# Optimization experiments

Measured on AMD Instinct MI355X. Metric: run time of the kernel, lower is better.

## Reference

```python
import jax, jax.numpy as jnp
import numpy as np
from itertools import permutations

BLOCK = 64  # GroupLinear block_size


def _dist_bucket_table():
    # replicates self.distance: log2-style bucketing of token distances [0,1024)
    t = np.zeros(1024, dtype=np.int32)
    for i, th in enumerate([2, 4, 8, 16, 32, 64, 128, 256, 512]):
        t[th:] = i + 1
    return jnp.asarray(t)


def setup_inputs() -> dict:
    key = jax.random.key(0)
    ks = jax.random.split(key, 12)
    B, S, H, NH = 4, 512, 768, 12
    E, TAG, TE, TD, R = 24, 7, 20, 20, 97
    DIN = 2 * H + TE + TD
    hidden_state = jax.random.normal(ks[0], (B, S, H), jnp.float32)
    attention = jax.random.uniform(ks[1], (B, NH, S, S), jnp.float32)
    attention_mask = jnp.ones((B, S), jnp.float32)
    head = jnp.sort(jax.random.randint(ks[2], (B, E), 0, S), axis=-1)
    tail = jnp.sort(jax.random.randint(ks[3], (B, E), 0, S), axis=-1)
    entity_type = jax.random.randint(ks[4], (B, E), 0, TAG)
    type_table = jax.random.normal(ks[5], (TAG, TE), jnp.float32) * 0.02
    dis_table = jax.random.normal(ks[6], (20, TD), jnp.float32) * 0.02
    Wh = jax.random.normal(ks[7], (DIN, H), jnp.float32) * (1.0 / np.sqrt(DIN))
    bh = jnp.zeros((H,), jnp.float32)
    Wt = jax.random.normal(ks[8], (DIN, H), jnp.float32) * (1.0 / np.sqrt(DIN))
    bt = jnp.zeros((H,), jnp.float32)
    # GroupLinear weight reshaped to [n_blocks, BLOCK, BLOCK, R]
    clsW = jax.random.normal(ks[9], (H // BLOCK, BLOCK, BLOCK, R), jnp.float32) * (1.0 / np.sqrt(H * BLOCK))
    clsb = jnp.zeros((R,), jnp.float32)
    return dict(hidden_state=hidden_state, attention=attention,
                attention_mask=attention_mask, head=head, tail=tail,
                entity_type=entity_type, type_table=type_table,
                dis_table=dis_table, Wh=Wh, bh=bh, Wt=Wt, bt=bt,
                clsW=clsW, clsb=clsb)


def reference(hidden_state, attention, attention_mask, head, tail, entity_type,
              type_table, dis_table, Wh, bh, Wt, bt, clsW, clsb):
    E = head.shape[1]
    hts = jnp.asarray(list(permutations(range(E), 2)), dtype=jnp.int32)  # [P,2]
    i0, i1 = hts[:, 0], hts[:, 1]
    dtab = _dist_bucket_table()
    att = attention.sum(axis=1)  # [B,S,S] sum over heads

    def per_sample(h, a, m, hd, tl, et):
        # h:[S,H] a:[S,S] m:[S] hd,tl,et:[E]
        ent_feat = (h[hd] + h[tl]) * 0.5          # [E,H]
        ent_att = (a[hd] + a[tl]) * 0.5           # [E,S]
        ent_tf = type_table[et]                   # [E,TE]
        head_f, tail_f = ent_feat[i0], ent_feat[i1]      # [P,H]
        ht_att = ent_att[i0] * ent_att[i1] * m[None, :]  # [P,S]
        head_ty, tail_ty = ent_tf[i0], ent_tf[i1]        # [P,TE]
        d = dtab[jnp.abs(tl[i0] - hd[i1])]               # [P]
        ht_dist = dis_table[d]                           # [P,TD]
        ht_att = ht_att / (ht_att.sum(-1, keepdims=True) + 1e-20)
        ht_info = ht_att @ h                             # [P,H]
        all_h = jnp.concatenate([head_f, ht_info, head_ty, ht_dist], axis=-1)
        all_t = jnp.concatenate([tail_f, ht_info, tail_ty, ht_dist], axis=-1)
        return all_h, all_t

    all_h, all_t = jax.vmap(per_sample)(hidden_state, att, attention_mask,
                                        head, tail, entity_type)
    all_h = all_h.reshape(-1, all_h.shape[-1])  # [B*P, DIN]
    all_t = all_t.reshape(-1, all_t.shape[-1])
    h1 = jnp.tanh(all_h @ Wh + bh)              # [L,H]
    t1 = jnp.tanh(all_t @ Wt + bt)
    L, H = h1.shape
    nb = H // BLOCK
    x1 = h1.reshape(L, nb, BLOCK)
    x2 = t1.reshape(L, nb, BLOCK)
    # GroupLinear: per-block outer product then linear, fused as einsum
    logits = jnp.einsum('lnb,lnc,nbcr->lr', x1, x2, clsW) + clsb  # [L,R]
    return logits
```

## Files before the change

### kernel.cpp

```cpp
#include <hip/hip_runtime.h>
#include <hip/hip_bf16.h>
#include <math.h>

#define B_ 4
#define S_ 512
#define H_ 768
#define NH_ 12
#define E_ 24
#define TE_ 20
#define TD_ 20
#define R_ 97
#define DIN_ 1576
#define KPAD_ 1600
#define KS_MLP 50
#define KS_HTI 16
#define P_ 552
#define L_ 2208
#define NB_ 12
#define NF_ 7

typedef __bf16 bf16x8 __attribute__((ext_vector_type(8)));
typedef float f32x4 __attribute__((ext_vector_type(4)));

__device__ __forceinline__ unsigned short f2bf(float f) {
  union { float f; unsigned u; } c; c.f = f;
  unsigned r = c.u + 0x7FFF + ((c.u >> 16) & 1);
  return (unsigned short)(r >> 16);
}
__device__ __forceinline__ float bf2f(unsigned short b) {
  union { unsigned u; float f; } c; c.u = ((unsigned)b) << 16;
  return c.f;
}
__device__ __forceinline__ unsigned pk2(float a, float b) {
  return (unsigned)f2bf(a) | ((unsigned)f2bf(b) << 16);
}
__device__ __forceinline__ void gload_lds16(const uint4* g, uint4* l) {
  __builtin_amdgcn_global_load_lds(
      (const __attribute__((address_space(1))) unsigned*)(const void*)g,
      (__attribute__((address_space(3))) unsigned*)(void*)l, 16, 0, 0);
}

__global__ void ent_prep(const float* __restrict__ attn, const float* __restrict__ hs,
                         const int* __restrict__ head, const int* __restrict__ tail,
                         float* __restrict__ ent_att, float* __restrict__ ent_feat) {
  int be = blockIdx.x;
  int b = be / E_;
  int hd = head[be], tl = tail[be];
  int tid = threadIdx.x;
  const float* abase = attn + (size_t)b * NH_ * S_ * S_;
  for (int s = tid; s < S_; s += 256) {
    float acc = 0.f;
#pragma unroll
    for (int nh = 0; nh < NH_; ++nh) {
      const float* ap = abase + (size_t)nh * S_ * S_;
      acc += ap[(size_t)hd * S_ + s] + ap[(size_t)tl * S_ + s];
    }
    ent_att[(size_t)be * S_ + s] = 0.5f * acc;
  }
  const float* hb = hs + (size_t)b * S_ * H_;
  for (int k = tid; k < H_; k += 256) {
    ent_feat[(size_t)be * H_ + k] = 0.5f * (hb[(size_t)hd * H_ + k] + hb[(size_t)tl * H_ + k]);
  }
}

__global__ void pair_att(const float* __restrict__ ent_att, const float* __restrict__ mask,
                         const int* __restrict__ head, const int* __restrict__ tail,
                         const int* __restrict__ etype,
                         float* __restrict__ ht_att, int* __restrict__ meta) {
  int l = blockIdx.x;
  int b = l / P_, p = l % P_;
  int i0 = p / (E_ - 1), rem = p % (E_ - 1);
  int i1 = rem + (rem >= i0 ? 1 : 0);
  int tid = threadIdx.x;
  if (tid == 0) {
    meta[0 * L_ + l] = b * E_ + i0;
    meta[1 * L_ + l] = b * E_ + i1;
    meta[2 * L_ + l] = etype[b * E_ + i0];
    meta[3 * L_ + l] = etype[b * E_ + i1];
    int d = abs(tail[b * E_ + i0] - head[b * E_ + i1]);
    int bk = (d >= 2) + (d >= 4) + (d >= 8) + (d >= 16) + (d >= 32) +
             (d >= 64) + (d >= 128) + (d >= 256) + (d >= 512);
    meta[4 * L_ + l] = bk;
  }
  const float* a0 = ent_att + (size_t)(b * E_ + i0) * S_;
  const float* a1 = ent_att + (size_t)(b * E_ + i1) * S_;
  const float* m = mask + (size_t)b * S_;
  float v0 = a0[tid] * a1[tid] * m[tid];
  float v1 = a0[tid + 256] * a1[tid + 256] * m[tid + 256];
  float loc = v0 + v1;
  for (int o = 32; o > 0; o >>= 1) loc += __shfl_down(loc, o, 64);
  __shared__ float red[4];
  if ((tid & 63) == 0) red[tid >> 6] = loc;
  __syncthreads();
  float tot = red[0] + red[1] + red[2] + red[3];
  float inv = 1.f / (tot + 1e-20f);
  ht_att[(size_t)l * S_ + tid] = v0 * inv;
  ht_att[(size_t)l * S_ + tid + 256] = v1 * inv;
}

__global__ void pack_hs(const float* __restrict__ hs, uint4* __restrict__ hsP) {
  int u = blockIdx.x * 256 + threadIdx.x;
  if (u >= B_ * KS_HTI * 48 * 64) return;
  int lane = u & 63;
  int t = u >> 6;
  int nt16 = t % 48;
  int t2 = t / 48;
  int ks = t2 % KS_HTI;
  int b = t2 / KS_HTI;
  int n = nt16 * 16 + (lane & 15);
  int k0 = ks * 32 + ((lane >> 4) << 3);
  const float* src = hs + (size_t)b * S_ * H_;
  unsigned w[4];
#pragma unroll
  for (int q = 0; q < 4; ++q) {
    int k = k0 + 2 * q;
    w[q] = pk2(src[(size_t)k * H_ + n], src[(size_t)(k + 1) * H_ + n]);
  }
  uint4 o; o.x = w[0]; o.y = w[1]; o.z = w[2]; o.w = w[3];
  hsP[u] = o;
}

__global__ void pack_Wmlp(const float* __restrict__ Wh, const float* __restrict__ Wt,
                          uint4* __restrict__ WpH, uint4* __restrict__ WpT) {
  int u = blockIdx.x * 256 + threadIdx.x;
  if (u >= KS_MLP * 48 * 64) return;
  const float* W = blockIdx.y ? Wt : Wh;
  uint4* Wp = blockIdx.y ? WpT : WpH;
  int lane = u & 63;
  int t = u >> 6;
  int nt16 = t % 48;
  int ks = t / 48;
  int n = nt16 * 16 + (lane & 15);
  int k0 = ks * 32 + ((lane >> 4) << 3);
  unsigned w[4];
#pragma unroll
  for (int q = 0; q < 4; ++q) {
    int k = k0 + 2 * q;
    float v0 = (k < DIN_) ? W[(size_t)k * H_ + n] : 0.f;
    float v1 = (k + 1 < DIN_) ? W[(size_t)(k + 1) * H_ + n] : 0.f;
    w[q] = pk2(v0, v1);
  }
  uint4 o; o.x = w[0]; o.y = w[1]; o.z = w[2]; o.w = w[3];
  Wp[u] = o;
}

__global__ __launch_bounds__(256) void htinfo_mfma(
    const float* __restrict__ htatt, const uint4* __restrict__ hsP,
    float* __restrict__ htinfo) {
  int b = blockIdx.z;
  int m0 = blockIdx.x * 64;
  int n0 = blockIdx.y * 64;
  int tid = threadIdx.x;
  int wave = tid >> 6, lane = tid & 63;
  int wm = wave & 1, wn = wave >> 1;
  __shared__ __align__(16) unsigned short Ash[2][2048];
  __shared__ __align__(16) uint4 Bsh[2][256];

  int amt = tid >> 6, alane = tid & 63;
  int arow = m0 + amt * 16 + (alane & 15);
  bool rowok = arow < P_;
  const float* ap = htatt + ((size_t)b * P_ + (rowok ? arow : 0)) * S_;
  int akoff = (alane >> 4) << 3;
  int nt0 = n0 >> 4;

  f32x4 acc[2][2];
#pragma unroll
  for (int i = 0; i < 2; ++i)
#pragma unroll
    for (int j = 0; j < 2; ++j) acc[i][j] = (f32x4){0.f, 0.f, 0.f, 0.f};

  auto stageB = [&](int ks, int buf) {
    const uint4* gs = hsP + ((size_t)(b * KS_HTI + ks) * 48 + nt0 + wave) * 64 + lane;
    gload_lds16(gs, &Bsh[buf][wave * 64]);
  };
  auto gatherA = [&](int ks, uint4& d) {
    if (!rowok) { d.x = d.y = d.z = d.w = 0; return; }
    int k = ks * 32 + akoff;
    float4 v0 = *(const float4*)(ap + k);
    float4 v1 = *(const float4*)(ap + k + 4);
    d.x = pk2(v0.x, v0.y); d.y = pk2(v0.z, v0.w);
    d.z = pk2(v1.x, v1.y); d.w = pk2(v1.z, v1.w);
  };

  {
    stageB(0, 0);
    uint4 aU; gatherA(0, aU);
    *(uint4*)&Ash[0][tid * 8] = aU;
  }
  __syncthreads();

  for (int ks = 0; ks < KS_HTI; ++ks) {
    int cur = ks & 1, nxt = cur ^ 1;
    bool more = (ks + 1 < KS_HTI);
    uint4 aN;
    if (more) {
      stageB(ks + 1, nxt);
      gatherA(ks + 1, aN);
    }
    bf16x8 af[2], bf[2];
#pragma unroll
    for (int mf = 0; mf < 2; ++mf)
      af[mf] = *(const bf16x8*)&Ash[cur][((wm * 2 + mf) * 64 + lane) * 8];
#pragma unroll
    for (int nf = 0; nf < 2; ++nf)
      bf[nf] = *(const bf16x8*)&Bsh[cur][(wn * 2 + nf) * 64 + lane];
#pragma unroll
    for (int nf = 0; nf < 2; ++nf)
#pragma unroll
      for (int mf = 0; mf < 2; ++mf)
        acc[mf][nf] = __builtin_amdgcn_mfma_f32_16x16x32_bf16(af[mf], bf[nf], acc[mf][nf], 0, 0, 0);
    if (more)
      *(uint4*)&Ash[nxt][tid * 8] = aN;
    __syncthreads();
  }

#pragma unroll
  for (int mf = 0; mf < 2; ++mf)
#pragma unroll
    for (int nf = 0; nf < 2; ++nf) {
      int n = n0 + (wn * 2 + nf) * 16 + (lane & 15);
#pragma unroll
      for (int reg = 0; reg < 4; ++reg) {
        int l = m0 + (wm * 2 + mf) * 16 + ((lane >> 4) << 2) + reg;
        if (l < P_)
          htinfo[((size_t)b * P_ + l) * H_ + n] = acc[mf][nf][reg];
      }
    }
}

__global__ __launch_bounds__(256) void mlp_mfma(
    const float* __restrict__ ent_feat, const float* __restrict__ ht_info,
    const float* __restrict__ ttab, const float* __restrict__ dtab,
    const int* __restrict__ meta,
    const uint4* __restrict__ Wp_h, const uint4* __restrict__ Wp_t,
    const float* __restrict__ bh, const float* __restrict__ bt,
    float* __restrict__ h1, float* __restrict__ t1) {
  int half = blockIdx.z;
  const uint4* Wp = half ? Wp_t : Wp_h;
  const float* bias = half ? bt : bh;
  float* out = half ? t1 : h1;
  const int* feat_row = meta + half * L_;
  const int* type_row = meta + (2 + half) * L_;
  const int* distb = meta + 4 * L_;

  int l0 = blockIdx.x * 64;
  int n0 = blockIdx.y * 64;
  int tid = threadIdx.x;
  int wave = tid >> 6, lane = tid & 63;
  int wm = wave & 1, wn = wave >> 1;
  __shared__ __align__(16) unsigned short Ash[2][2048];
  __shared__ __align__(16) uint4 Bsh[2][256];

  int amt = tid >> 6, alane = tid & 63;
  int arow = l0 + amt * 16 + (alane & 15);
  bool rowok = arow < L_;
  int frow = 0, trow = 0, db = 0;
  if (rowok) { frow = feat_row[arow]; trow = type_row[arow]; db = distb[arow]; }
  const float* efp = ent_feat + (size_t)frow * H_;
  const float* hip_ = ht_info + (size_t)arow * H_;
  int akoff = (alane >> 4) << 3;
  int nt0 = n0 >> 4;

  f32x4 acc[2][2];
#pragma unroll
  for (int i = 0; i < 2; ++i)
#pragma unroll
    for (int j = 0; j < 2; ++j) acc[i][j] = (f32x4){0.f, 0.f, 0.f, 0.f};

  auto stageB = [&](int ks, int buf) {
    const uint4* gs = Wp + ((size_t)ks * 48 + nt0 + wave) * 64 + lane;
    gload_lds16(gs, &Bsh[buf][wave * 64]);
  };
  auto gatherA = [&](int ks, uint4& d) {
    int k = ks * 32 + akoff;
    if (!rowok) { d.x = d.y = d.z = d.w = 0; return; }
    if (k < 768) {
      float4 v0 = *(const float4*)(efp + k);
      float4 v1 = *(const float4*)(efp + k + 4);
      d.x = pk2(v0.x, v0.y); d.y = pk2(v0.z, v0.w);
      d.z = pk2(v1.x, v1.y); d.w = pk2(v1.z, v1.w);
    } else if (k < 1536) {
      float4 v0 = *(const float4*)(hip_ + k - 768);
      float4 v1 = *(const float4*)(hip_ + k - 764);
      d.x = pk2(v0.x, v0.y); d.y = pk2(v0.z, v0.w);
      d.z = pk2(v1.x, v1.y); d.w = pk2(v1.z, v1.w);
    } else {
      float v[8];
#pragma unroll
      for (int j = 0; j < 8; ++j) {
        int e = k + j;
        v[j] = (e < 1556) ? ttab[trow * TE_ + (e - 1536)]
             : (e < 1576) ? dtab[db * TD_ + (e - 1556)] : 0.f;
      }
      d.x = pk2(v[0], v[1]); d.y = pk2(v[2], v[3]);
      d.z = pk2(v[4], v[5]); d.w = pk2(v[6], v[7]);
    }
  };

  {
    stageB(0, 0);
    uint4 aU; gatherA(0, aU);
    *(uint4*)&Ash[0][tid * 8] = aU;
  }
  __syncthreads();

  for (int ks = 0; ks < KS_MLP; ++ks) {
    int cur = ks & 1, nxt = cur ^ 1;
    bool more = (ks + 1 < KS_MLP);
    uint4 aN;
    if (more) {
      stageB(ks + 1, nxt);
      gatherA(ks + 1, aN);
    }
    bf16x8 af[2], bf[2];
#pragma unroll
    for (int mf = 0; mf < 2; ++mf)
      af[mf] = *(const bf16x8*)&Ash[cur][((wm * 2 + mf) * 64 + lane) * 8];
#pragma unroll
    for (int nf = 0; nf < 2; ++nf)
      bf[nf] = *(const bf16x8*)&Bsh[cur][(wn * 2 + nf) * 64 + lane];
#pragma unroll
    for (int nf = 0; nf < 2; ++nf)
#pragma unroll
      for (int mf = 0; mf < 2; ++mf)
        acc[mf][nf] = __builtin_amdgcn_mfma_f32_16x16x32_bf16(af[mf], bf[nf], acc[mf][nf], 0, 0, 0);
    if (more)
      *(uint4*)&Ash[nxt][tid * 8] = aN;
    __syncthreads();
  }

#pragma unroll
  for (int mf = 0; mf < 2; ++mf)
#pragma unroll
    for (int nf = 0; nf < 2; ++nf) {
      int n = n0 + (wn * 2 + nf) * 16 + (lane & 15);
      float bv = bias[n];
#pragma unroll
      for (int reg = 0; reg < 4; ++reg) {
        int l = l0 + (wm * 2 + mf) * 16 + ((lane >> 4) << 2) + reg;
        if (l < L_)
          out[(size_t)l * H_ + n] = tanhf(acc[mf][nf][reg] + bv);
      }
    }
}

__global__ void pack_w(const float* __restrict__ clsW, uint4* __restrict__ Wfrag) {
  int nb = blockIdx.x;
  __shared__ float Wls[64][98];
  int tid = threadIdx.x;
  const float* src = clsW + (size_t)nb * 64 * R_;
  for (int idx = tid; idx < 64 * R_; idx += 256) {
    Wls[idx / R_][idx % R_] = src[idx];
  }
  __syncthreads();
  for (int u = tid; u < 896; u += 256) {
    int nf = u >> 7;
    int kc = (u >> 6) & 1;
    int lane = u & 63;
    int r = (lane & 15) + 16 * nf;
    unsigned w[4];
#pragma unroll
    for (int q = 0; q < 4; ++q) {
      int c0 = ((lane >> 4) << 3) + 2 * q + 32 * kc;
      float v0 = (r < R_) ? Wls[c0][r] : 0.f;
      float v1 = (r < R_) ? Wls[c0 + 1][r] : 0.f;
      w[q] = (unsigned)f2bf(v0) | ((unsigned)f2bf(v1) << 16);
    }
    uint4 o; o.x = w[0]; o.y = w[1]; o.z = w[2]; o.w = w[3];
    Wfrag[(size_t)nb * 896 + u] = o;
  }
}

__global__ __launch_bounds__(256) void bilinear_mfma(
    const float* __restrict__ h1, const float* __restrict__ t1,
    const uint4* __restrict__ Wfrag, float* __restrict__ part) {
  int n = blockIdx.y;
  int l0 = blockIdx.x * 64;
  int tid = threadIdx.x;
  int wave = tid >> 6, lane = tid & 63;
  int wm = wave & 1, kh = wave >> 1;
  __shared__ __align__(16) uint4 Wl[2][2][896];
  __shared__ unsigned short x1s[64][64];

  for (int i = tid; i < 1024; i += 256) {
    int l = i >> 4, bq = (i & 15) * 4;
    float4 v = make_float4(0, 0, 0, 0);
    if (l0 + l < L_) v = *(const float4*)(h1 + (size_t)(l0 + l) * H_ + n * 64 + bq);
    x1s[bq + 0][l] = f2bf(v.x);
    x1s[bq + 1][l] = f2bf(v.y);
    x1s[bq + 2][l] = f2bf(v.z);
    x1s[bq + 3][l] = f2bf(v.w);
  }

  float x2f[2][2][8];
#pragma unroll
  for (int mf = 0; mf < 2; ++mf) {
    int row = l0 + wm * 32 + mf * 16 + (lane & 15);
#pragma unroll
    for (int kc = 0; kc < 2; ++kc) {
      float4 v0 = make_float4(0, 0, 0, 0), v1 = v0;
      if (row < L_) {
        const float* p = t1 + (size_t)row * H_ + n * 64 + kc * 32 + ((lane >> 4) << 3);
        v0 = *(const float4*)p;
        v1 = *(const float4*)(p + 4);
      }
      x2f[mf][kc][0] = v0.x; x2f[mf][kc][1] = v0.y;
      x2f[mf][kc][2] = v0.z; x2f[mf][kc][3] = v0.w;
      x2f[mf][kc][4] = v1.x; x2f[mf][kc][5] = v1.y;
      x2f[mf][kc][6] = v1.z; x2f[mf][kc][7] = v1.w;
    }
  }

  f32x4 acc[2][NF_];
#pragma unroll
  for (int mf = 0; mf < 2; ++mf)
#pragma unroll
    for (int nf = 0; nf < NF_; ++nf)
      acc[mf][nf] = (f32x4){0.f, 0.f, 0.f, 0.f};

  const uint4* gbase = Wfrag + (size_t)n * 64 * 896;
  auto stage = [&](int b, int buf) {
    const uint4* gs = gbase + (size_t)b * 896 + (wm * 7) * 64 + lane;
#pragma unroll
    for (int r = 0; r < 7; ++r)
      gload_lds16(gs + r * 64, &Wl[kh][buf][(wm * 7 + r) * 64]);
  };

  stage(kh * 32, 0);
  __syncthreads();

  for (int s = 0; s < 32; ++s) {
    int b = kh * 32 + s;
    int cur = s & 1, nxt = cur ^ 1;
    if (s + 1 < 32) stage(b + 1, nxt);
    bf16x8 afr[2][2];
#pragma unroll
    for (int mf = 0; mf < 2; ++mf) {
      float x1v = bf2f(x1s[b][wm * 32 + mf * 16 + (lane & 15)]);
#pragma unroll
      for (int kc = 0; kc < 2; ++kc)
#pragma unroll
        for (int j = 0; j < 8; ++j)
          afr[mf][kc][j] = (__bf16)(x1v * x2f[mf][kc][j]);
    }
#pragma unroll
    for (int nf = 0; nf < NF_; ++nf) {
#pragma unroll
      for (int kc = 0; kc < 2; ++kc) {
        bf16x8 bfr = *(const bf16x8*)&Wl[kh][cur][(nf * 2 + kc) * 64 + lane];
#pragma unroll
        for (int mf = 0; mf < 2; ++mf)
          acc[mf][nf] = __builtin_amdgcn_mfma_f32_16x16x32_bf16(
              afr[mf][kc], bfr, acc[mf][nf], 0, 0, 0);
      }
    }
    __syncthreads();
  }

  float* red = (float*)&Wl[0][0][0];
  int rbase = (wm * 64 + lane) * 68;
  if (kh == 1) {
#pragma unroll
    for (int mf = 0; mf < 2; ++mf)
#pragma unroll
      for (int nf = 0; nf < NF_; ++nf)
        *(f32x4*)&red[rbase + (mf * NF_ + nf) * 4] = acc[mf][nf];
  }
  __syncthreads();
  if (kh == 0) {
#pragma unroll
    for (int mf = 0; mf < 2; ++mf)
#pragma unroll
      for (int nf = 0; nf < NF_; ++nf)
        acc[mf][nf] += *(const f32x4*)&red[rbase + (mf * NF_ + nf) * 4];
#pragma unroll
    for (int mf = 0; mf < 2; ++mf) {
#pragma unroll
      for (int nf = 0; nf < NF_; ++nf) {
        int r = nf * 16 + (lane & 15);
        if (r < R_) {
#pragma unroll
          for (int reg = 0; reg < 4; ++reg) {
            int l = l0 + wm * 32 + mf * 16 + ((lane >> 4) << 2) + reg;
            if (l < L_)
              part[((size_t)n * L_ + l) * R_ + r] = acc[mf][nf][reg];
          }
        }
      }
    }
  }
}

__global__ void reduce_logits(const float* __restrict__ part, const float* __restrict__ clsb,
                              float* __restrict__ out) {
  int idx = blockIdx.x * 256 + threadIdx.x;
  if (idx < L_ * R_) {
    int r = idx % R_;
    float s = clsb[r];
#pragma unroll
    for (int nn = 0; nn < NB_; ++nn) s += part[(size_t)nn * L_ * R_ + idx];
    out[idx] = s;
  }
}

extern "C" void kernel_launch(void* const* d_in, const int* in_sizes, int n_in,
                              void* d_out, int out_size, void* d_ws, size_t ws_size,
                              hipStream_t stream) {
  const float* hs   = (const float*)d_in[0];
  const float* attn = (const float*)d_in[1];
  const float* mask = (const float*)d_in[2];
  const int*   head = (const int*)d_in[3];
  const int*   tail = (const int*)d_in[4];
  const int*   etyp = (const int*)d_in[5];
  const float* ttab = (const float*)d_in[6];
  const float* dtab = (const float*)d_in[7];
  const float* Wh   = (const float*)d_in[8];
  const float* bh   = (const float*)d_in[9];
  const float* Wt   = (const float*)d_in[10];
  const float* bt   = (const float*)d_in[11];
  const float* clsW = (const float*)d_in[12];
  const float* clsb = (const float*)d_in[13];
  float* out = (float*)d_out;

  float* ws = (float*)d_ws;
  float* ent_att  = ws; ws += (size_t)B_ * E_ * S_;
  float* ent_feat = ws; ws += (size_t)B_ * E_ * H_;
  float* ht_att   = ws; ws += (size_t)L_ * S_;
  float* ht_info  = ws; ws += (size_t)L_ * H_;
  float* h1       = ws; ws += (size_t)L_ * H_;
  float* t1       = ws; ws += (size_t)L_ * H_;
  float* part     = ws; ws += (size_t)NB_ * L_ * R_;
  int* meta = (int*)ws;

  uint4* Wpack_h = (uint4*)ht_att;
  uint4* Wpack_t = (uint4*)part;
  uint4* hsPack  = (uint4*)(part + (size_t)1048576);
  uint4* Wfrag   = (uint4*)ht_att;

  ent_prep<<<B_ * E_, 256, 0, stream>>>(attn, hs, head, tail, ent_att, ent_feat);
  pair_att<<<L_, 256, 0, stream>>>(ent_att, mask, head, tail, etyp, ht_att, meta);
  pack_hs<<<(B_ * KS_HTI * 48 * 64) / 256, 256, 0, stream>>>(hs, hsPack);
  htinfo_mfma<<<dim3(9, 12, B_), 256, 0, stream>>>(ht_att, hsPack, ht_info);
  pack_Wmlp<<<dim3((KS_MLP * 48 * 64) / 256, 2), 256, 0, stream>>>(Wh, Wt, Wpack_h, Wpack_t);
  mlp_mfma<<<dim3(35, 12, 2), 256, 0, stream>>>(ent_feat, ht_info, ttab, dtab, meta,
      Wpack_h, Wpack_t, bh, bt, h1, t1);
  pack_w<<<NB_ * 64, 256, 0, stream>>>(clsW, Wfrag);
  bilinear_mfma<<<dim3(35, NB_), 256, 0, stream>>>(h1, t1, Wfrag, part);
  reduce_logits<<<(L_ * R_ + 255) / 256, 256, 0, stream>>>(part, clsb, out);
}
```

Before: 141.9 us.

## Pre-pack MLP activations to bf16 fragments and deepen GEMM k-steps

Adds a pack_allx kernel that gathers the concatenated head/tail features and converts them to bf16 MFMA fragment layout once. The MLP GEMM can then stage both A and B with async global-to-LDS loads instead of gathering and converting in-loop. Both the htinfo and MLP GEMMs now process 64-wide k-steps per barrier (two MFMA k-chunks), halving loop iterations and syncs. Workspace buffers stop aliasing and get dedicated regions. The cost is an extra kernel launch plus a write and re-read of the packed activation buffer.

Result: faster. 125.8 us (-11.4%).

```diff
diff --git a/kernel.cpp b/kernel.cpp
--- a/kernel.cpp
+++ b/kernel.cpp
@@ -13,6 +13,7 @@
 #define DIN_ 1576
 #define KPAD_ 1600
 #define KS_MLP 50
+#define MF_MLP 140
 #define KS_HTI 16
 #define P_ 552
 #define L_ 2208
@@ -144,144 +145,31 @@
   Wp[u] = o;
 }
 
-__global__ __launch_bounds__(256) void htinfo_mfma(
-    const float* __restrict__ htatt, const uint4* __restrict__ hsP,
-    float* __restrict__ htinfo) {
-  int b = blockIdx.z;
-  int m0 = blockIdx.x * 64;
-  int n0 = blockIdx.y * 64;
-  int tid = threadIdx.x;
-  int wave = tid >> 6, lane = tid & 63;
-  int wm = wave & 1, wn = wave >> 1;
-  __shared__ __align__(16) unsigned short Ash[2][2048];
-  __shared__ __align__(16) uint4 Bsh[2][256];
-
-  int amt = tid >> 6, alane = tid & 63;
-  int arow = m0 + amt * 16 + (alane & 15);
-  bool rowok = arow < P_;
-  const float* ap = htatt + ((size_t)b * P_ + (rowok ? arow : 0)) * S_;
-  int akoff = (alane >> 4) << 3;
-  int nt0 = n0 >> 4;
-
-  f32x4 acc[2][2];
-#pragma unroll
-  for (int i = 0; i < 2; ++i)
-#pragma unroll
-    for (int j = 0; j < 2; ++j) acc[i][j] = (f32x4){0.f, 0.f, 0.f, 0.f};
-
-  auto stageB = [&](int ks, int buf) {
-    const uint4* gs = hsP + ((size_t)(b * KS_HTI + ks) * 48 + nt0 + wave) * 64 + lane;
-    gload_lds16(gs, &Bsh[buf][wave * 64]);
-  };
-  auto gatherA = [&](int ks, uint4& d) {
-    if (!rowok) { d.x = d.y = d.z = d.w = 0; return; }
-    int k = ks * 32 + akoff;
-    float4 v0 = *(const float4*)(ap + k);
-    float4 v1 = *(const float4*)(ap + k + 4);
-    d.x = pk2(v0.x, v0.y); d.y = pk2(v0.z, v0.w);
-    d.z = pk2(v1.x, v1.y); d.w = pk2(v1.z, v1.w);
-  };
-
-  {
-    stageB(0, 0);
-    uint4 aU; gatherA(0, aU);
-    *(uint4*)&Ash[0][tid * 8] = aU;
-  }
-  __syncthreads();
-
-  for (int ks = 0; ks < KS_HTI; ++ks) {
-    int cur = ks & 1, nxt = cur ^ 1;
-    bool more = (ks + 1 < KS_HTI);
-    uint4 aN;
-    if (more) {
-      stageB(ks + 1, nxt);
-      gatherA(ks + 1, aN);
-    }
-    bf16x8 af[2], bf[2];
-#pragma unroll
-    for (int mf = 0; mf < 2; ++mf)
-      af[mf] = *(const bf16x8*)&Ash[cur][((wm * 2 + mf) * 64 + lane) * 8];
-#pragma unroll
-    for (int nf = 0; nf < 2; ++nf)
-      bf[nf] = *(const bf16x8*)&Bsh[cur][(wn * 2 + nf) * 64 + lane];
-#pragma unroll
-    for (int nf = 0; nf < 2; ++nf)
-#pragma unroll
-      for (int mf = 0; mf < 2; ++mf)
-        acc[mf][nf] = __builtin_amdgcn_mfma_f32_16x16x32_bf16(af[mf], bf[nf], acc[mf][nf], 0, 0, 0);
-    if (more)
-      *(uint4*)&Ash[nxt][tid * 8] = aN;
-    __syncthreads();
-  }
-
-#pragma unroll
-  for (int mf = 0; mf < 2; ++mf)
-#pragma unroll
-    for (int nf = 0; nf < 2; ++nf) {
-      int n = n0 + (wn * 2 + nf) * 16 + (lane & 15);
-#pragma unroll
-      for (int reg = 0; reg < 4; ++reg) {
-        int l = m0 + (wm * 2 + mf) * 16 + ((lane >> 4) << 2) + reg;
-        if (l < P_)
-          htinfo[((size_t)b * P_ + l) * H_ + n] = acc[mf][nf][reg];
-      }
-    }
-}
-
-__global__ __launch_bounds__(256) void mlp_mfma(
-    const float* __restrict__ ent_feat, const float* __restrict__ ht_info,
-    const float* __restrict__ ttab, const float* __restrict__ dtab,
-    const int* __restrict__ meta,
-    const uint4* __restrict__ Wp_h, const uint4* __restrict__ Wp_t,
-    const float* __restrict__ bh, const float* __restrict__ bt,
-    float* __restrict__ h1, float* __restrict__ t1) {
-  int half = blockIdx.z;
-  const uint4* Wp = half ? Wp_t : Wp_h;
-  const float* bias = half ? bt : bh;
-  float* out = half ? t1 : h1;
-  const int* feat_row = meta + half * L_;
-  const int* type_row = meta + (2 + half) * L_;
-  const int* distb = meta + 4 * L_;
-
-  int l0 = blockIdx.x * 64;
-  int n0 = blockIdx.y * 64;
-  int tid = threadIdx.x;
-  int wave = tid >> 6, lane = tid & 63;
-  int wm = wave & 1, wn = wave >> 1;
-  __shared__ __align__(16) unsigned short Ash[2][2048];
-  __shared__ __align__(16) uint4 Bsh[2][256];
-
-  int amt = tid >> 6, alane = tid & 63;
-  int arow = l0 + amt * 16 + (alane & 15);
-  bool rowok = arow < L_;
-  int frow = 0, trow = 0, db = 0;
-  if (rowok) { frow = feat_row[arow]; trow = type_row[arow]; db = distb[arow]; }
-  const float* efp = ent_feat + (size_t)frow * H_;
-  const float* hip_ = ht_info + (size_t)arow * H_;
-  int akoff = (alane >> 4) << 3;
-  int nt0 = n0 >> 4;
-
-  f32x4 acc[2][2];
-#pragma unroll
-  for (int i = 0; i < 2; ++i)
-#pragma unroll
-    for (int j = 0; j < 2; ++j) acc[i][j] = (f32x4){0.f, 0.f, 0.f, 0.f};
-
-  auto stageB = [&](int ks, int buf) {
-    const uint4* gs = Wp + ((size_t)ks * 48 + nt0 + wave) * 64 + lane;
-    gload_lds16(gs, &Bsh[buf][wave * 64]);
-  };
-  auto gatherA = [&](int ks, uint4& d) {
-    int k = ks * 32 + akoff;
-    if (!rowok) { d.x = d.y = d.z = d.w = 0; return; }
+__global__ void pack_allx(const float* __restrict__ ent_feat, const float* __restrict__ ht_info,
+                          const float* __restrict__ ttab, const float* __restrict__ dtab,
+                          const int* __restrict__ meta,
+                          uint4* __restrict__ axH, uint4* __restrict__ axT) {
+  int idx = blockIdx.x * 256 + threadIdx.x;
+  int lane = idx & 63;
+  int unit = idx >> 6;
+  int half = unit / (MF_MLP * KS_MLP);
+  int rem = unit % (MF_MLP * KS_MLP);
+  int mf = rem / KS_MLP, ks = rem % KS_MLP;
+  int row = mf * 16 + (lane & 15);
+  int k = ks * 32 + ((lane >> 4) << 3);
+  uint4 d; d.x = d.y = d.z = d.w = 0;
+  if (row < L_) {
+    int frow = meta[half * L_ + row];
+    int trow = meta[(2 + half) * L_ + row];
+    int db = meta[4 * L_ + row];
     if (k < 768) {
-      float4 v0 = *(const float4*)(efp + k);
-      float4 v1 = *(const float4*)(efp + k + 4);
+      const float* p = ent_feat + (size_t)frow * H_ + k;
+      float4 v0 = *(const float4*)p, v1 = *(const float4*)(p + 4);
       d.x = pk2(v0.x, v0.y); d.y = pk2(v0.z, v0.w);
       d.z = pk2(v1.x, v1.y); d.w = pk2(v1.z, v1.w);
     } else if (k < 1536) {
-      float4 v0 = *(const float4*)(hip_ + k - 768);
-      float4 v1 = *(const float4*)(hip_ + k - 764);
+      const float* p = ht_info + (size_t)row * H_ + (k - 768);
+      float4 v0 = *(const float4*)p, v1 = *(const float4*)(p + 4);
       d.x = pk2(v0.x, v0.y); d.y = pk2(v0.z, v0.w);
       d.z = pk2(v1.x, v1.y); d.w = pk2(v1.z, v1.w);
     } else {
@@ -295,37 +183,164 @@
       d.x = pk2(v[0], v[1]); d.y = pk2(v[2], v[3]);
       d.z = pk2(v[4], v[5]); d.w = pk2(v[6], v[7]);
     }
+  }
+  (half ? axT : axH)[(size_t)rem * 64 + lane] = d;
+}
+
+__global__ __launch_bounds__(256) void htinfo_mfma(
+    const float* __restrict__ htatt, const uint4* __restrict__ hsP,
+    float* __restrict__ htinfo) {
+  int b = blockIdx.z;
+  int m0 = blockIdx.x * 64;
+  int nt0 = blockIdx.y * 4;
+  int tid = threadIdx.x;
+  int wave = tid >> 6, lane = tid & 63;
+  int wm = wave & 1, wn = wave >> 1;
+  __shared__ __align__(16) uint4 Ash[2][512];
+  __shared__ __align__(16) uint4 Bsh[2][512];
+
+  f32x4 acc[2][2];
+#pragma unroll
+  for (int i = 0; i < 2; ++i)
+#pragma unroll
+    for (int j = 0; j < 2; ++j) acc[i][j] = (f32x4){0.f, 0.f, 0.f, 0.f};
+
+  auto stageB = [&](int s, int buf) {
+#pragma unroll
+    for (int i = 0; i < 2; ++i) {
+      int c = wave * 2 + i;
+      int ntl = c >> 1, kslot = c & 1;
+      gload_lds16(hsP + ((size_t)(b * KS_HTI + s * 2 + kslot) * 48 + nt0 + ntl) * 64 + lane,
+                  &Bsh[buf][c * 64]);
+    }
   };
+  auto gatherA = [&](int s, int c, uint4& d) {
+    int mfl = c >> 1, kslot = c & 1;
+    int row = m0 + mfl * 16 + (lane & 15);
+    if (row >= P_) { d.x = d.y = d.z = d.w = 0; return; }
+    int k = s * 64 + kslot * 32 + ((lane >> 4) << 3);
+    const float* p = htatt + ((size_t)b * P_ + row) * S_ + k;
+    float4 v0 = *(const float4*)p, v1 = *(const float4*)(p + 4);
+    d.x = pk2(v0.x, v0.y); d.y = pk2(v0.z, v0.w);
+    d.z = pk2(v1.x, v1.y); d.w = pk2(v1.z, v1.w);
+  };
 
   {
+    uint4 a0_, a1_;
+    gatherA(0, wave, a0_); gatherA(0, wave + 4, a1_);
+    Ash[0][wave * 64 + lane] = a0_;
+    Ash[0][(wave + 4) * 64 + lane] = a1_;
     stageB(0, 0);
-    uint4 aU; gatherA(0, aU);
-    *(uint4*)&Ash[0][tid * 8] = aU;
   }
   __syncthreads();
 
-  for (int ks = 0; ks < KS_MLP; ++ks) {
-    int cur = ks & 1, nxt = cur ^ 1;
-    bool more = (ks + 1 < KS_MLP);
-    uint4 aN;
+  for (int s = 0; s < 8; ++s) {
+    int cur = s & 1, nxt = cur ^ 1;
+    bool more = (s + 1 < 8);
+    uint4 aN0, aN1;
     if (more) {
-      stageB(ks + 1, nxt);
-      gatherA(ks + 1, aN);
-    }
-    bf16x8 af[2], bf[2];
+      stageB(s + 1, nxt);
+      gatherA(s + 1, wave, aN0); gatherA(s + 1, wave + 4, aN1);
+    }
+    bf16x8 af[2][2], bf[2][2];
 #pragma unroll
     for (int mf = 0; mf < 2; ++mf)
-      af[mf] = *(const bf16x8*)&Ash[cur][((wm * 2 + mf) * 64 + lane) * 8];
+#pragma unroll
+      for (int kc = 0; kc < 2; ++kc)
+        af[mf][kc] = *(const bf16x8*)&Ash[cur][((wm * 2 + mf) * 2 + kc) * 64 + lane];
 #pragma unroll
     for (int nf = 0; nf < 2; ++nf)
-      bf[nf] = *(const bf16x8*)&Bsh[cur][(wn * 2 + nf) * 64 + lane];
+#pragma unroll
+      for (int kc = 0; kc < 2; ++kc)
+        bf[nf][kc] = *(const bf16x8*)&Bsh[cur][((wn * 2 + nf) * 2 + kc) * 64 + lane];
+#pragma unroll
+    for (int kc = 0; kc < 2; ++kc)
+#pragma unroll
+      for (int nf = 0; nf < 2; ++nf)
+#pragma unroll
+        for (int mf = 0; mf < 2; ++mf)
+          acc[mf][nf] = __builtin_amdgcn_mfma_f32_16x16x32_bf16(af[mf][kc], bf[nf][kc], acc[mf][nf], 0, 0, 0);
+    if (more) {
+      Ash[nxt][wave * 64 + lane] = aN0;
+      Ash[nxt][(wave + 4) * 64 + lane] = aN1;
+    }
+    __syncthreads();
+  }
+
+#pragma unroll
+  for (int mf = 0; mf < 2; ++mf)
+#pragma unroll
+    for (int nf = 0; nf < 2; ++nf) {
+      int n = nt0 * 16 + (wn * 2 + nf) * 16 + (lane & 15);
+#pragma unroll
+      for (int reg = 0; reg < 4; ++reg) {
+        int l = m0 + (wm * 2 + mf) * 16 + ((lane >> 4) << 2) + reg;
+        if (l < P_)
+          htinfo[((size_t)b * P_ + l) * H_ + n] = acc[mf][nf][reg];
+      }
+    }
+}
+
+__global__ __launch_bounds__(256) void mlp_mfma(
+    const uint4* __restrict__ Apk_h, const uint4* __restrict__ Apk_t,
+    const uint4* __restrict__ Wp_h, const uint4* __restrict__ Wp_t,
+    const float* __restrict__ bh, const float* __restrict__ bt,
+    float* __restrict__ h1, float* __restrict__ t1) {
+  int half = blockIdx.z;
+  const uint4* Apk = half ? Apk_t : Apk_h;
+  const uint4* Wp = half ? Wp_t : Wp_h;
+  const float* bias = half ? bt : bh;
+  float* out = half ? t1 : h1;
+  int mf0 = blockIdx.x * 4;
+  int nt0 = blockIdx.y * 4;
+  int tid = threadIdx.x;
+  int wave = tid >> 6, lane = tid & 63;
+  int wm = wave & 1, wn = wave >> 1;
+  __shared__ __align__(16) uint4 Ash[2][512];
+  __shared__ __align__(16) uint4 Bsh[2][512];
+
+  f32x4 acc[2][2];
+#pragma unroll
+  for (int i = 0; i < 2; ++i)
+#pragma unroll
+    for (int j = 0; j < 2; ++j) acc[i][j] = (f32x4){0.f, 0.f, 0.f, 0.f};
+
+  auto stage = [&](int s, int buf) {
+#pragma unroll
+    for (int i = 0; i < 2; ++i) {
+      int c = wave * 2 + i;
+      int cl = c >> 1, kslot = c & 1;
+      gload_lds16(Apk + ((size_t)(mf0 + cl) * KS_MLP + s * 2 + kslot) * 64 + lane,
+                  &Ash[buf][c * 64]);
+      gload_lds16(Wp + ((size_t)(s * 2 + kslot) * 48 + nt0 + cl) * 64 + lane,
+                  &Bsh[buf][c * 64]);
+    }
+  };
+
+  stage(0, 0);
+  __syncthreads();
+
+  for (int s = 0; s < 25; ++s) {
+    int cur = s & 1, nxt = cur ^ 1;
+    if (s + 1 < 25) stage(s + 1, nxt);
+    bf16x8 af[2][2], bf[2][2];
+#pragma unroll
+    for (int mf = 0; mf < 2; ++mf)
+#pragma unroll
+      for (int kc = 0; kc < 2; ++kc)
+        af[mf][kc] = *(const bf16x8*)&Ash[cur][((wm * 2 + mf) * 2 + kc) * 64 + lane];
 #pragma unroll
     for (int nf = 0; nf < 2; ++nf)
 #pragma unroll
-      for (int mf = 0; mf < 2; ++mf)
-        acc[mf][nf] = __builtin_amdgcn_mfma_f32_16x16x32_bf16(af[mf], bf[nf], acc[mf][nf], 0, 0, 0);
-    if (more)
-      *(uint4*)&Ash[nxt][tid * 8] = aN;
+      for (int kc = 0; kc < 2; ++kc)
+        bf[nf][kc] = *(const bf16x8*)&Bsh[cur][((wn * 2 + nf) * 2 + kc) * 64 + lane];
+#pragma unroll
+    for (int kc = 0; kc < 2; ++kc)
+#pragma unroll
+      for (int nf = 0; nf < 2; ++nf)
+#pragma unroll
+        for (int mf = 0; mf < 2; ++mf)
+          acc[mf][nf] = __builtin_amdgcn_mfma_f32_16x16x32_bf16(af[mf][kc], bf[nf][kc], acc[mf][nf], 0, 0, 0);
     __syncthreads();
   }
 
@@ -333,11 +348,11 @@
   for (int mf = 0; mf < 2; ++mf)
 #pragma unroll
     for (int nf = 0; nf < 2; ++nf) {
-      int n = n0 + (wn * 2 + nf) * 16 + (lane & 15);
+      int n = nt0 * 16 + (wn * 2 + nf) * 16 + (lane & 15);
       float bv = bias[n];
 #pragma unroll
       for (int reg = 0; reg < 4; ++reg) {
-        int l = l0 + (wm * 2 + mf) * 16 + ((lane >> 4) << 2) + reg;
+        int l = (mf0 + wm * 2 + mf) * 16 + ((lane >> 4) << 2) + reg;
         if (l < L_)
           out[(size_t)l * H_ + n] = tanhf(acc[mf][nf][reg] + bv);
       }
@@ -530,19 +545,22 @@
   float* h1       = ws; ws += (size_t)L_ * H_;
   float* t1       = ws; ws += (size_t)L_ * H_;
   float* part     = ws; ws += (size_t)NB_ * L_ * R_;
+  uint4* Wpack_h  = (uint4*)ws; ws += (size_t)KS_MLP * 48 * 64 * 4;
+  uint4* Wpack_t  = (uint4*)ws; ws += (size_t)KS_MLP * 48 * 64 * 4;
+  uint4* hsPack   = (uint4*)ws; ws += (size_t)B_ * KS_HTI * 48 * 64 * 4;
+  uint4* Wfrag    = (uint4*)ws; ws += (size_t)NB_ * 64 * 896 * 4;
+  uint4* allx_h   = (uint4*)ws; ws += (size_t)MF_MLP * KS_MLP * 64 * 4;
+  uint4* allx_t   = (uint4*)ws; ws += (size_t)MF_MLP * KS_MLP * 64 * 4;
   int* meta = (int*)ws;
-
-  uint4* Wpack_h = (uint4*)ht_att;
-  uint4* Wpack_t = (uint4*)part;
-  uint4* hsPack  = (uint4*)(part + (size_t)1048576);
-  uint4* Wfrag   = (uint4*)ht_att;
 
   ent_prep<<<B_ * E_, 256, 0, stream>>>(attn, hs, head, tail, ent_att, ent_feat);
   pair_att<<<L_, 256, 0, stream>>>(ent_att, mask, head, tail, etyp, ht_att, meta);
   pack_hs<<<(B_ * KS_HTI * 48 * 64) / 256, 256, 0, stream>>>(hs, hsPack);
   htinfo_mfma<<<dim3(9, 12, B_), 256, 0, stream>>>(ht_att, hsPack, ht_info);
   pack_Wmlp<<<dim3((KS_MLP * 48 * 64) / 256, 2), 256, 0, stream>>>(Wh, Wt, Wpack_h, Wpack_t);
-  mlp_mfma<<<dim3(35, 12, 2), 256, 0, stream>>>(ent_feat, ht_info, ttab, dtab, meta,
+  pack_allx<<<(2 * MF_MLP * KS_MLP * 64) / 256, 256, 0, stream>>>(
+      ent_feat, ht_info, ttab, dtab, meta, allx_h, allx_t);
+  mlp_mfma<<<dim3(35, 12, 2), 256, 0, stream>>>(allx_h, allx_t,
       Wpack_h, Wpack_t, bh, bt, h1, t1);
   pack_w<<<NB_ * 64, 256, 0, stream>>>(clsW, Wfrag);
   bilinear_mfma<<<dim3(35, NB_), 256, 0, stream>>>(h1, t1, Wfrag, part);
```
